# Kernel tuning notes

Measured on AMD Instinct MI355X. Metric: run time of the kernel, lower is better.

The kernel has to match this reference:

```python
import jax, jax.numpy as jnp
import numpy as np

NUM_HEADS = 8
HIDDEN = 256


def _coattention(qf, rf, Wq, bq, Wk, bk, Wv, bv, Wo, bo, rel_emb):
    # qf, rf: (b, c, h, w); attention is axial over the height axis per width column.
    b, c, h, w = qf.shape
    T = rel_emb.shape[0]  # 2*max(h,w)-1
    q_in = qf.reshape(b, c, h * w).transpose(0, 2, 1)  # b (hw) c
    r_in = rf.reshape(b, c, h * w).transpose(0, 2, 1)
    q = (q_in @ Wq + bq).reshape(b, h, w, NUM_HEADS, HIDDEN).transpose(0, 3, 1, 2, 4)  # b n h w c
    k = (r_in @ Wk + bk).reshape(b, h, w, NUM_HEADS, HIDDEN).transpose(0, 3, 1, 2, 4)
    v = (r_in @ Wv + bv).reshape(b, h, w, NUM_HEADS, HIDDEN).transpose(0, 3, 1, 2, 4)
    scores = jnp.einsum('bnhwc,bnkwc->bnhwk', q, k)
    # relative index table: idx[i, j] = j - i, wrapped like torch negative indexing
    idx_h = (jnp.arange(h)[None, :] - jnp.arange(h)[:, None]) % T  # (h, h)
    idx_w = (jnp.arange(w)[None, :] - jnp.arange(w)[:, None]) % T  # (w, w); h == w required
    rel_h = rel_emb[idx_h]  # (h, h, c)
    rel_w = rel_emb[idx_w]  # (w, w, c)
    scores = scores + jnp.einsum('bnhwc,hkc->bnhwk', q, rel_h)
    scores = scores + jnp.einsum('bnhwc,wkc->bnhwk', q, rel_w)
    probs = jax.nn.softmax(scores / np.float32(np.sqrt(HIDDEN)), axis=-1)
    att = jnp.einsum('bnhwk,bnkwc->bnhwc', probs, v)
    out = att.transpose(0, 2, 3, 1, 4).reshape(b, h * w, NUM_HEADS * HIDDEN)  # b (hw) (n c)
    out = out @ Wo + bo
    return out.transpose(0, 2, 1).reshape(b, c, h, w)


def setup_inputs() -> dict:
    key = jax.random.key(0)
    ks = jax.random.split(key, 8)
    B, C, H, W = 4, 2048, 32, 32
    s = np.float32(0.02)
    return {
        'left_features': jax.random.normal(ks[0], (B, C, H, W), jnp.float32),
        'right_features': jax.random.normal(ks[1], (B, C, H, W), jnp.float32),
        'Wq': jax.random.normal(ks[2], (C, C), jnp.float32) * s,
        'bq': jnp.zeros((C,), jnp.float32),
        'Wk': jax.random.normal(ks[3], (C, C), jnp.float32) * s,
        'bk': jnp.zeros((C,), jnp.float32),
        'Wv': jax.random.normal(ks[4], (C, C), jnp.float32) * s,
        'bv': jnp.zeros((C,), jnp.float32),
        'Wo': jax.random.normal(ks[5], (C, C), jnp.float32) * s,
        'bo': jnp.zeros((C,), jnp.float32),
        'rel_emb': jax.random.normal(ks[6], (2 * max(H, W) - 1, HIDDEN), jnp.float32),
    }


def reference(left_features, right_features, Wq, bq, Wk, bk, Wv, bv, Wo, bo, rel_emb):
    weighted_r = _coattention(left_features, right_features, Wq, bq, Wk, bk, Wv, bv, Wo, bo, rel_emb)
    weighted_l = _coattention(right_features, left_features, Wq, bq, Wk, bk, Wv, bv, Wo, bo, rel_emb)
    left_attended = jnp.concatenate([left_features, weighted_r], axis=1)
    right_attended = jnp.concatenate([right_features, weighted_l], axis=1)
    return (left_attended, right_attended)
```

## Files before the change

kernel.cpp:

```cpp
#include <hip/hip_runtime.h>
#include <hip/hip_bf16.h>

typedef __attribute__((ext_vector_type(8))) short bf16x8;
typedef __attribute__((ext_vector_type(4))) float f32x4;

#define MFMA16(a, b, c) __builtin_amdgcn_mfma_f32_16x16x32_bf16((a), (b), (c), 0, 0, 0)

typedef __attribute__((address_space(1))) const void gconst_t;
typedef __attribute__((address_space(3))) void lds_t;
__device__ __forceinline__ void gload16(const void* gp, void* lp) {
    __builtin_amdgcn_global_load_lds((gconst_t*)gp, (lds_t*)lp, 16, 0, 0);
}

#define BAR() asm volatile("s_barrier" ::: "memory")
#define VMCNT4() asm volatile("s_waitcnt vmcnt(4)" ::: "memory")
#define DRAIN() asm volatile("s_waitcnt vmcnt(0) lgkmcnt(0)" ::: "memory")
#define PRIO1() __builtin_amdgcn_s_setprio(1)
#define PRIO0() __builtin_amdgcn_s_setprio(0)
#define SCHED0() __builtin_amdgcn_sched_barrier(0)

__global__ void transpose_x(const float* __restrict__ in, __hip_bfloat16* __restrict__ out,
                            float* __restrict__ copy_out) {
    __shared__ float tile[32][33];
    int r0 = blockIdx.y * 32, c0 = blockIdx.x * 32;
    size_t zoff = (size_t)blockIdx.z * 2048 * 1024;
    const float* ib = in + zoff;
    __hip_bfloat16* ob = out + zoff;
    float* cb = copy_out + (size_t)blockIdx.z * 4194304;
    int tx = threadIdx.x, ty = threadIdx.y;
#pragma unroll
    for (int i = ty; i < 32; i += 8) {
        float v = ib[(size_t)(r0 + i) * 1024 + c0 + tx];
        tile[i][tx] = v;
        cb[(size_t)(r0 + i) * 1024 + c0 + tx] = v;
    }
    __syncthreads();
#pragma unroll
    for (int i = ty; i < 32; i += 8)
        ob[(size_t)(c0 + i) * 2048 + r0 + tx] = __float2bfloat16(tile[tx][i]);
}

struct TArgs {
    const float* src[4];
    __hip_bfloat16* dst[4];
};
__global__ void transpose_w4(TArgs ta) {
    __shared__ float tile[32][33];
    const int z = blockIdx.z;
    const float* __restrict__ ib = ta.src[z];
    __hip_bfloat16* __restrict__ ob = ta.dst[z];
    int r0 = blockIdx.y * 32, c0 = blockIdx.x * 32;
    int tx = threadIdx.x, ty = threadIdx.y;
#pragma unroll
    for (int i = ty; i < 32; i += 8)
        tile[i][tx] = ib[(size_t)(r0 + i) * 2048 + c0 + tx];
    __syncthreads();
#pragma unroll
    for (int i = ty; i < 32; i += 8)
        ob[(size_t)(c0 + i) * 2048 + r0 + tx] = __float2bfloat16(tile[tx][i]);
}

__global__ void conv_rel(const float* __restrict__ rel, __hip_bfloat16* __restrict__ relb) {
    int i = blockIdx.x * 256 + threadIdx.x;
    if (i < 64 * 256) {
        int r = i >> 8;
        relb[i] = __float2bfloat16(r < 63 ? rel[i] : 0.f);
    }
}

struct GArgs {
    const __hip_bfloat16* A[6];
    const __hip_bfloat16* B[6];
    void* C[6];
    const float* bias[6];
};

template <int MODE>
__global__ __launch_bounds__(512, 2) void gemm8p(GArgs ga, int N, int K,
                                                 float* __restrict__ dout) {
    __shared__ __align__(16) char smem[131072];

    const int gx = gridDim.x, gy = gridDim.y;
    int lid = blockIdx.x + gx * (blockIdx.y + gy * blockIdx.z);
    const int nwg = gx * gy * gridDim.z;
    int swz = (lid & 7) * (nwg >> 3) + (lid >> 3);
    const int z = swz / (gx * gy);
    int rem = swz - z * (gx * gy);
    const int by = rem / gx;
    const int bx = rem - by * gx;

    const __hip_bfloat16* __restrict__ A = ga.A[z];
    const __hip_bfloat16* __restrict__ B = ga.B[z];
    const float* __restrict__ bias = ga.bias[z];
    const int row0 = by * 256, col0 = bx * 256;

    const int tid = threadIdx.x;
    const int wave = tid >> 6, lane = tid & 63;
    const int l15 = lane & 15, lg = lane >> 4;
    const int wm = wave >> 2, wn = wave & 3;

    const int srow = tid >> 3;
    const int sch = (tid & 7) ^ (srow & 7);
    const int xr = (l15 & 7) << 4;
    const int off0 = (lg * 16) ^ xr;
    const int off1 = (64 + lg * 16) ^ xr;
    const int arow = wm * 16384;
    const int brow = 32768 + (wn >> 1) * 16384;
    const int bloc = (wn & 1) * 64;

    f32x4 acc[8][4] = {};
    bf16x8 alo[4][2], ahi[4][2], bhi[2][2], blo0[2][2], blo1[2][2];

    const int NT = K >> 6;
    const int NI = NT >> 1;

    auto STAGE = [&](const __hip_bfloat16* base, int rowb, int T, int bufc, int isB, int h) {
#pragma unroll
        for (int L = 0; L < 2; ++L) {
            const __hip_bfloat16* g =
                base + (size_t)(rowb + h * 128 + L * 64 + srow) * K + T * 64 + sch * 8;
            gload16(g, smem + bufc * 65536 + isB * 32768 + h * 16384 + L * 8192 + wave * 1024);
        }
    };
    auto LDA = [&](int bufc, int mf, int ks) {
        return *(const bf16x8*)(smem + bufc * 65536 + arow + (mf * 16 + l15) * 128 +
                                (ks ? off1 : off0));
    };
    auto LDB = [&](int bufc, int nf, int ks) {
        return *(const bf16x8*)(smem + bufc * 65536 + brow + (bloc + nf * 16 + l15) * 128 +
                                (ks ? off1 : off0));
    };

#define READ_ALO(BUF)                                  \
    _Pragma("unroll") for (int mf = 0; mf < 4; ++mf) { \
        alo[mf][0] = LDA(BUF, mf, 0);                  \
        alo[mf][1] = LDA(BUF, mf, 1);                  \
    }
#define READ_AHI(BUF)                                  \
    _Pragma("unroll") for (int mf = 0; mf < 4; ++mf) { \
        ahi[mf][0] = LDA(BUF, 4 + mf, 0);              \
        ahi[mf][1] = LDA(BUF, 4 + mf, 1);              \
    }
#define READ_BHI(BUF)                                  \
    _Pragma("unroll") for (int nf = 0; nf < 2; ++nf) { \
        bhi[nf][0] = LDB(BUF, 2 + nf, 0);              \
        bhi[nf][1] = LDB(BUF, 2 + nf, 1);              \
    }
#define READ_BLO(BUF, DST)                             \
    _Pragma("unroll") for (int nf = 0; nf < 2; ++nf) { \
        DST[nf][0] = LDB(BUF, nf, 0);                  \
        DST[nf][1] = LDB(BUF, nf, 1);                  \
    }
#define MQ(AR, MOFF, NOFF, BR)                                          \
    SCHED0();                                                           \
    PRIO1();                                                            \
    _Pragma("unroll") for (int mf = 0; mf < 4; ++mf)                    \
    _Pragma("unroll") for (int nf = 0; nf < 2; ++nf) {                  \
        acc[(MOFF) + mf][(NOFF) + nf] =                                 \
            MFMA16(AR[mf][0], BR[nf][0], acc[(MOFF) + mf][(NOFF) + nf]); \
        acc[(MOFF) + mf][(NOFF) + nf] =                                 \
            MFMA16(AR[mf][1], BR[nf][1], acc[(MOFF) + mf][(NOFF) + nf]); \
    }                                                                   \
    PRIO0();

    STAGE(B, col0, 0, 0, 1, 0);
    STAGE(A, row0, 0, 0, 0, 0);
    STAGE(A, row0, 0, 0, 0, 1);
    STAGE(B, col0, 0, 0, 1, 1);
    STAGE(B, col0, 1, 1, 1, 0);
    STAGE(A, row0, 1, 1, 0, 0);
    VMCNT4();
    BAR();
    READ_ALO(0);
    READ_BLO(0, blo0);

#pragma unroll 1
    for (int i = 0; i < NI; ++i) {
        const int t = 2 * i;
        const int T2 = (t + 2 < NT) ? t + 2 : t;
        const int T3 = (t + 3 < NT) ? t + 3 : t + 1;
        STAGE(A, row0, t + 1, 1, 0, 1);
        BAR();
        READ_BHI(0);
        MQ(alo, 0, 0, blo0);

        STAGE(B, col0, t + 1, 1, 1, 1);
        BAR();
        READ_AHI(0);
        MQ(alo, 0, 2, bhi);

        STAGE(B, col0, T2, 0, 1, 0);
        BAR();
        MQ(ahi, 4, 2, bhi);

        STAGE(A, row0, T2, 0, 0, 0);
        VMCNT4();
        BAR();
        READ_ALO(1);
        READ_BLO(1, blo1);
        MQ(ahi, 4, 0, blo0);

        STAGE(A, row0, T2, 0, 0, 1);
        BAR();
        READ_BHI(1);
        MQ(alo, 0, 0, blo1);

        STAGE(B, col0, T2, 0, 1, 1);
        BAR();
        READ_AHI(1);
        MQ(alo, 0, 2, bhi);

        STAGE(B, col0, T3, 1, 1, 0);
        BAR();
        MQ(ahi, 4, 2, bhi);

        STAGE(A, row0, T3, 1, 0, 0);
        VMCNT4();
        BAR();
        READ_ALO(0);
        READ_BLO(0, blo0);
        MQ(ahi, 4, 0, blo1);
    }
    DRAIN();

    if (MODE == 0) {
        __hip_bfloat16* __restrict__ C = (__hip_bfloat16*)ga.C[z];
#pragma unroll
        for (int mf = 0; mf < 8; ++mf) {
            int m = row0 + wm * 128 + mf * 16 + lg * 4;
#pragma unroll
            for (int nf = 0; nf < 4; ++nf) {
                int n = col0 + wn * 64 + nf * 16 + l15;
                float bv = bias[n];
#pragma unroll
                for (int r = 0; r < 4; ++r)
                    C[(size_t)(m + r) * N + n] = __float2bfloat16(acc[mf][nf][r] + bv);
            }
        }
    } else {
        float* __restrict__ OB = dout + (size_t)z * 16777216;
#pragma unroll
        for (int mf = 0; mf < 8; ++mf) {
            int n0 = row0 + wm * 128 + mf * 16 + lg * 4;
#pragma unroll
            for (int nf = 0; nf < 4; ++nf) {
                int m = col0 + wn * 64 + nf * 16 + l15;
                size_t base = (size_t)(m >> 10) * 4194304 + (size_t)(m & 1023);
#pragma unroll
                for (int r = 0; r < 4; ++r) {
                    int n = n0 + r;
                    OB[base + (size_t)(2048 + n) * 1024] = acc[mf][nf][r] + bias[n];
                }
            }
        }
    }
#undef READ_ALO
#undef READ_AHI
#undef READ_BHI
#undef READ_BLO
#undef MQ
}

__global__ __launch_bounds__(256, 2) void attn_kernel(
    const __hip_bfloat16* __restrict__ Qa, const __hip_bfloat16* __restrict__ Ka,
    const __hip_bfloat16* __restrict__ Va, const __hip_bfloat16* __restrict__ Qb,
    const __hip_bfloat16* __restrict__ Kb, const __hip_bfloat16* __restrict__ Vb,
    const __hip_bfloat16* __restrict__ relb, __hip_bfloat16* __restrict__ Oa,
    __hip_bfloat16* __restrict__ Ob) {
    const int w = blockIdx.x;
    const int nh = blockIdx.y;
    const int zb = blockIdx.z;
    const int dir = zb >> 2, b = zb & 3;
    const __hip_bfloat16* __restrict__ Q = dir ? Qb : Qa;
    const __hip_bfloat16* __restrict__ K = dir ? Kb : Ka;
    const __hip_bfloat16* __restrict__ V = dir ? Vb : Va;
    __hip_bfloat16* __restrict__ O = dir ? Ob : Oa;

    __shared__ __align__(16) __hip_bfloat16 vt[256 * 40];
    __shared__ float ssc[32 * 32];
    __shared__ float es[32 * 64];
    __shared__ __align__(16) __hip_bfloat16 ps[32 * 32];

    const int tid = threadIdx.x;
    const int lane = tid & 63, wave = tid >> 6;
    const int l15 = lane & 15, lg = lane >> 4;
    const int mt = wave >> 1, nt = wave & 1;

    const size_t rowbase = ((size_t)b * 1024 + w) * 2048 + (size_t)nh * 256;

    for (int i = 0; i < 32; ++i) {
        int e = i * 256 + tid;
        int hk = e >> 8, c = e & 255;
        vt[c * 40 + hk] = V[rowbase + (size_t)hk * 65536 + c];
    }

    f32x4 sacc = {}, e0 = {}, e1 = {};
#pragma unroll
    for (int k8 = 0; k8 < 256; k8 += 32) {
        bf16x8 af = *(const bf16x8*)&Q[rowbase + (size_t)(mt * 16 + l15) * 65536 + k8 + lg * 8];
        bf16x8 bf = *(const bf16x8*)&K[rowbase + (size_t)(nt * 16 + l15) * 65536 + k8 + lg * 8];
        bf16x8 r0 = *(const bf16x8*)&relb[(size_t)(nt * 32 + l15) * 256 + k8 + lg * 8];
        bf16x8 r1 = *(const bf16x8*)&relb[(size_t)(nt * 32 + 16 + l15) * 256 + k8 + lg * 8];
        sacc = MFMA16(af, bf, sacc);
        e0 = MFMA16(af, r0, e0);
        e1 = MFMA16(af, r1, e1);
    }
#pragma unroll
    for (int r = 0; r < 4; ++r) {
        int row = mt * 16 + lg * 4 + r;
        ssc[row * 32 + nt * 16 + l15] = sacc[r];
        es[row * 64 + nt * 32 + l15] = e0[r];
        es[row * 64 + nt * 32 + 16 + l15] = e1[r];
    }
    __syncthreads();

    {
        int h = tid >> 3, sub = tid & 7;
        float v4[4];
        float mx = -1e30f;
#pragma unroll
        for (int i = 0; i < 4; ++i) {
            int k = sub * 4 + i;
            int dh = k - h; if (dh < 0) dh += 63;
            int dw = k - w; if (dw < 0) dw += 63;
            float s = (ssc[h * 32 + k] + es[h * 64 + dh] + es[h * 64 + dw]) * 0.0625f;
            v4[i] = s;
            mx = fmaxf(mx, s);
        }
        mx = fmaxf(mx, __shfl_xor(mx, 1));
        mx = fmaxf(mx, __shfl_xor(mx, 2));
        mx = fmaxf(mx, __shfl_xor(mx, 4));
        float sum = 0.f;
#pragma unroll
        for (int i = 0; i < 4; ++i) {
            v4[i] = __expf(v4[i] - mx);
            sum += v4[i];
        }
        sum += __shfl_xor(sum, 1);
        sum += __shfl_xor(sum, 2);
        sum += __shfl_xor(sum, 4);
        float inv = 1.f / sum;
#pragma unroll
        for (int i = 0; i < 4; ++i) ps[h * 32 + sub * 4 + i] = __float2bfloat16(v4[i] * inv);
    }
    __syncthreads();

    bf16x8 paf = *(const bf16x8*)&ps[(mt * 16 + l15) * 32 + lg * 8];
#pragma unroll
    for (int j = 0; j < 8; ++j) {
        int ct = nt * 8 + j;
        bf16x8 bv = *(const bf16x8*)&vt[(size_t)(ct * 16 + l15) * 40 + lg * 8];
        f32x4 oacc = {};
        oacc = MFMA16(paf, bv, oacc);
#pragma unroll
        for (int r = 0; r < 4; ++r) {
            int hh = mt * 16 + lg * 4 + r;
            O[rowbase + (size_t)hh * 65536 + ct * 16 + l15] = __float2bfloat16(oacc[r]);
        }
    }
}

extern "C" void kernel_launch(void* const* d_in, const int* in_sizes, int n_in, void* d_out,
                              int out_size, void* d_ws, size_t ws_size, hipStream_t stream) {
    const float* Xl = (const float*)d_in[0];
    const float* Xr = (const float*)d_in[1];
    const float* Wq = (const float*)d_in[2];
    const float* bq = (const float*)d_in[3];
    const float* Wk = (const float*)d_in[4];
    const float* bk = (const float*)d_in[5];
    const float* Wv = (const float*)d_in[6];
    const float* bv = (const float*)d_in[7];
    const float* Wo = (const float*)d_in[8];
    const float* bo = (const float*)d_in[9];
    const float* rel = (const float*)d_in[10];
    float* out = (float*)d_out;

    char* ws = (char*)d_ws;
    size_t off = 0;
    auto nxt = [&](size_t bytes) {
        void* p = ws + off;
        off += bytes;
        return p;
    };
    __hip_bfloat16* Xbl = (__hip_bfloat16*)nxt(16777216);
    __hip_bfloat16* Xbr = (__hip_bfloat16*)nxt(16777216);
    __hip_bfloat16* Wtq = (__hip_bfloat16*)nxt(8388608);
    __hip_bfloat16* Wtk = (__hip_bfloat16*)nxt(8388608);
    __hip_bfloat16* Wtv = (__hip_bfloat16*)nxt(8388608);
    __hip_bfloat16* Wto = (__hip_bfloat16*)nxt(8388608);
    __hip_bfloat16* relb = (__hip_bfloat16*)nxt(32768);
    __hip_bfloat16* Ql = (__hip_bfloat16*)nxt(16777216);
    __hip_bfloat16* Kl = (__hip_bfloat16*)nxt(16777216);
    __hip_bfloat16* Vl = (__hip_bfloat16*)nxt(16777216);
    __hip_bfloat16* Qr = (__hip_bfloat16*)nxt(16777216);
    __hip_bfloat16* Kr = (__hip_bfloat16*)nxt(16777216);
    __hip_bfloat16* Vr = (__hip_bfloat16*)nxt(16777216);
    __hip_bfloat16* At0 = Xbl;
    __hip_bfloat16* At1 = Xbr;

    dim3 tb(32, 8);
    transpose_x<<<dim3(32, 64, 4), tb, 0, stream>>>(Xl, Xbl, out);
    transpose_x<<<dim3(32, 64, 4), tb, 0, stream>>>(Xr, Xbr, out + 16777216);
    TArgs tw;
    tw.src[0] = Wq; tw.src[1] = Wk; tw.src[2] = Wv; tw.src[3] = Wo;
    tw.dst[0] = Wtq; tw.dst[1] = Wtk; tw.dst[2] = Wtv; tw.dst[3] = Wto;
    transpose_w4<<<dim3(64, 64, 4), tb, 0, stream>>>(tw);
    conv_rel<<<64, 256, 0, stream>>>(rel, relb);

    GArgs g1 = {};
    g1.A[0] = Xbl; g1.A[1] = Xbl; g1.A[2] = Xbl;
    g1.A[3] = Xbr; g1.A[4] = Xbr; g1.A[5] = Xbr;
    g1.B[0] = Wtq; g1.B[1] = Wtk; g1.B[2] = Wtv;
    g1.B[3] = Wtq; g1.B[4] = Wtk; g1.B[5] = Wtv;
    g1.C[0] = Ql; g1.C[1] = Kl; g1.C[2] = Vl;
    g1.C[3] = Qr; g1.C[4] = Kr; g1.C[5] = Vr;
    g1.bias[0] = bq; g1.bias[1] = bk; g1.bias[2] = bv;
    g1.bias[3] = bq; g1.bias[4] = bk; g1.bias[5] = bv;
    gemm8p<0><<<dim3(8, 16, 6), 512, 0, stream>>>(g1, 2048, 2048, nullptr);

    attn_kernel<<<dim3(32, 8, 8), 256, 0, stream>>>(Ql, Kr, Vr, Qr, Kl, Vl, relb, At0, At1);

    GArgs g2 = {};
    g2.A[0] = Wto; g2.A[1] = Wto;
    g2.B[0] = At0; g2.B[1] = At1;
    g2.bias[0] = bo; g2.bias[1] = bo;
    gemm8p<1><<<dim3(16, 8, 2), 512, 0, stream>>>(g2, 2048, 2048, out);
}
```

Before: 386.7 us.

## Load GEMM B operand directly from global into registers, stage only A in LDS

Restructures the GEMM main loop so that only the A tile is staged through LDS (halving shared memory to 64KB), while each wave loads its B fragments directly from global memory into registers, double-buffered across k-steps. The previous 8-phase interleaved schedule with partial vmcnt waits is replaced by a simpler per-tile window that issues the next loads, does LDS reads and MFMAs, then waits for all loads and barriers. This aims to cut LDS traffic and capacity and to simplify synchronisation. The costs are uncoalesced global B loads, duplicate B reads across waves (wm=0/1), a full vmcnt(0) stall each tile, and higher register pressure.

Result: slower. 488.5 us (+26.3%).

```diff
diff --git a/kernel.cpp b/kernel.cpp
--- a/kernel.cpp
+++ b/kernel.cpp
@@ -13,8 +13,7 @@
 }
 
 #define BAR() asm volatile("s_barrier" ::: "memory")
-#define VMCNT4() asm volatile("s_waitcnt vmcnt(4)" ::: "memory")
-#define DRAIN() asm volatile("s_waitcnt vmcnt(0) lgkmcnt(0)" ::: "memory")
+#define VMCNT0() asm volatile("s_waitcnt vmcnt(0)" ::: "memory")
 #define PRIO1() __builtin_amdgcn_s_setprio(1)
 #define PRIO0() __builtin_amdgcn_s_setprio(0)
 #define SCHED0() __builtin_amdgcn_sched_barrier(0)
@@ -78,7 +77,7 @@
 template <int MODE>
 __global__ __launch_bounds__(512, 2) void gemm8p(GArgs ga, int N, int K,
                                                  float* __restrict__ dout) {
-    __shared__ __align__(16) char smem[131072];
+    __shared__ __align__(16) char smem[65536];
 
     const int gx = gridDim.x, gy = gridDim.y;
     int lid = blockIdx.x + gx * (blockIdx.y + gy * blockIdx.z);
@@ -102,126 +101,78 @@
     const int srow = tid >> 3;
     const int sch = (tid & 7) ^ (srow & 7);
     const int xr = (l15 & 7) << 4;
-    const int off0 = (lg * 16) ^ xr;
-    const int off1 = (64 + lg * 16) ^ xr;
-    const int arow = wm * 16384;
-    const int brow = 32768 + (wn >> 1) * 16384;
-    const int bloc = (wn & 1) * 64;
+
+    const __hip_bfloat16* Bw = B + (size_t)(col0 + wn * 64) * K;
 
     f32x4 acc[8][4] = {};
-    bf16x8 alo[4][2], ahi[4][2], bhi[2][2], blo0[2][2], blo1[2][2];
+    bf16x8 bA[4][2], bB[4][2], a0[2][2], a1[2][2];
 
     const int NT = K >> 6;
-    const int NI = NT >> 1;
-
-    auto STAGE = [&](const __hip_bfloat16* base, int rowb, int T, int bufc, int isB, int h) {
-#pragma unroll
-        for (int L = 0; L < 2; ++L) {
+
+    auto STAGE = [&](int T, int bufsel) {
+#pragma unroll
+        for (int L = 0; L < 4; ++L) {
             const __hip_bfloat16* g =
-                base + (size_t)(rowb + h * 128 + L * 64 + srow) * K + T * 64 + sch * 8;
-            gload16(g, smem + bufc * 65536 + isB * 32768 + h * 16384 + L * 8192 + wave * 1024);
+                A + (size_t)(row0 + L * 64 + srow) * K + T * 64 + sch * 8;
+            gload16(g, smem + bufsel * 32768 + L * 8192 + wave * 1024);
         }
     };
-    auto LDA = [&](int bufc, int mf, int ks) {
-        return *(const bf16x8*)(smem + bufc * 65536 + arow + (mf * 16 + l15) * 128 +
-                                (ks ? off1 : off0));
+    auto BLOAD = [&](bf16x8 (&dst)[4][2], int T) {
+#pragma unroll
+        for (int nf = 0; nf < 4; ++nf)
+#pragma unroll
+            for (int ks = 0; ks < 2; ++ks)
+                dst[nf][ks] =
+                    *(const bf16x8*)&Bw[(size_t)(nf * 16 + l15) * K + T * 64 + ks * 32 + lg * 8];
     };
-    auto LDB = [&](int bufc, int nf, int ks) {
-        return *(const bf16x8*)(smem + bufc * 65536 + brow + (bloc + nf * 16 + l15) * 128 +
-                                (ks ? off1 : off0));
+    auto RDA = [&](bf16x8 (&dst)[2][2], int bufsel, int mf0) {
+#pragma unroll
+        for (int p = 0; p < 2; ++p)
+#pragma unroll
+            for (int ks = 0; ks < 2; ++ks) {
+                int row = wm * 128 + (mf0 + p) * 16 + l15;
+                dst[p][ks] = *(const bf16x8*)(smem + bufsel * 32768 + row * 128 +
+                                              ((ks * 64 + lg * 16) ^ xr));
+            }
     };
 
-#define READ_ALO(BUF)                                  \
-    _Pragma("unroll") for (int mf = 0; mf < 4; ++mf) { \
-        alo[mf][0] = LDA(BUF, mf, 0);                  \
-        alo[mf][1] = LDA(BUF, mf, 1);                  \
-    }
-#define READ_AHI(BUF)                                  \
-    _Pragma("unroll") for (int mf = 0; mf < 4; ++mf) { \
-        ahi[mf][0] = LDA(BUF, 4 + mf, 0);              \
-        ahi[mf][1] = LDA(BUF, 4 + mf, 1);              \
-    }
-#define READ_BHI(BUF)                                  \
-    _Pragma("unroll") for (int nf = 0; nf < 2; ++nf) { \
-        bhi[nf][0] = LDB(BUF, 2 + nf, 0);              \
-        bhi[nf][1] = LDB(BUF, 2 + nf, 1);              \
-    }
-#define READ_BLO(BUF, DST)                             \
-    _Pragma("unroll") for (int nf = 0; nf < 2; ++nf) { \
-        DST[nf][0] = LDB(BUF, nf, 0);                  \
-        DST[nf][1] = LDB(BUF, nf, 1);                  \
-    }
-#define MQ(AR, MOFF, NOFF, BR)                                          \
-    SCHED0();                                                           \
-    PRIO1();                                                            \
-    _Pragma("unroll") for (int mf = 0; mf < 4; ++mf)                    \
-    _Pragma("unroll") for (int nf = 0; nf < 2; ++nf) {                  \
-        acc[(MOFF) + mf][(NOFF) + nf] =                                 \
-            MFMA16(AR[mf][0], BR[nf][0], acc[(MOFF) + mf][(NOFF) + nf]); \
-        acc[(MOFF) + mf][(NOFF) + nf] =                                 \
-            MFMA16(AR[mf][1], BR[nf][1], acc[(MOFF) + mf][(NOFF) + nf]); \
-    }                                                                   \
-    PRIO0();
-
-    STAGE(B, col0, 0, 0, 1, 0);
-    STAGE(A, row0, 0, 0, 0, 0);
-    STAGE(A, row0, 0, 0, 0, 1);
-    STAGE(B, col0, 0, 0, 1, 1);
-    STAGE(B, col0, 1, 1, 1, 0);
-    STAGE(A, row0, 1, 1, 0, 0);
-    VMCNT4();
+#define MFMA2(AP, MOFF, BC)                                                       \
+    _Pragma("unroll") for (int p = 0; p < 2; ++p)                                 \
+    _Pragma("unroll") for (int nf = 0; nf < 4; ++nf) {                            \
+        acc[(MOFF) + p][nf] = MFMA16(AP[p][0], BC[nf][0], acc[(MOFF) + p][nf]);   \
+        acc[(MOFF) + p][nf] = MFMA16(AP[p][1], BC[nf][1], acc[(MOFF) + p][nf]);   \
+    }
+
+#define WINDOW(TT, BUFSEL, BC, BN)                            \
+    {                                                         \
+        const int tn = ((TT) + 1 < NT) ? (TT) + 1 : (TT);     \
+        STAGE(tn, (BUFSEL) ^ 1);                              \
+        BLOAD(BN, tn);                                        \
+        SCHED0();                                             \
+        RDA(a0, (BUFSEL), 0);                                 \
+        RDA(a1, (BUFSEL), 2);                                 \
+        PRIO1();                                              \
+        MFMA2(a0, 0, BC);                                     \
+        RDA(a0, (BUFSEL), 4);                                 \
+        MFMA2(a1, 2, BC);                                     \
+        RDA(a1, (BUFSEL), 6);                                 \
+        MFMA2(a0, 4, BC);                                     \
+        MFMA2(a1, 6, BC);                                     \
+        PRIO0();                                              \
+        VMCNT0();                                             \
+        BAR();                                                \
+    }
+
+    STAGE(0, 0);
+    BLOAD(bA, 0);
+    VMCNT0();
     BAR();
-    READ_ALO(0);
-    READ_BLO(0, blo0);
 
 #pragma unroll 1
-    for (int i = 0; i < NI; ++i) {
-        const int t = 2 * i;
-        const int T2 = (t + 2 < NT) ? t + 2 : t;
-        const int T3 = (t + 3 < NT) ? t + 3 : t + 1;
-        STAGE(A, row0, t + 1, 1, 0, 1);
-        BAR();
-        READ_BHI(0);
-        MQ(alo, 0, 0, blo0);
-
-        STAGE(B, col0, t + 1, 1, 1, 1);
-        BAR();
-        READ_AHI(0);
-        MQ(alo, 0, 2, bhi);
-
-        STAGE(B, col0, T2, 0, 1, 0);
-        BAR();
-        MQ(ahi, 4, 2, bhi);
-
-        STAGE(A, row0, T2, 0, 0, 0);
-        VMCNT4();
-        BAR();
-        READ_ALO(1);
-        READ_BLO(1, blo1);
-        MQ(ahi, 4, 0, blo0);
-
-        STAGE(A, row0, T2, 0, 0, 1);
-        BAR();
-        READ_BHI(1);
-        MQ(alo, 0, 0, blo1);
-
-        STAGE(B, col0, T2, 0, 1, 1);
-        BAR();
-        READ_AHI(1);
-        MQ(alo, 0, 2, bhi);
-
-        STAGE(B, col0, T3, 1, 1, 0);
-        BAR();
-        MQ(ahi, 4, 2, bhi);
-
-        STAGE(A, row0, T3, 1, 0, 0);
-        VMCNT4();
-        BAR();
-        READ_ALO(0);
-        READ_BLO(0, blo0);
-        MQ(ahi, 4, 0, blo1);
-    }
-    DRAIN();
+    for (int t = 0; t < NT; t += 2) {
+        WINDOW(t, 0, bA, bB);
+        WINDOW(t + 1, 1, bB, bA);
+    }
 
     if (MODE == 0) {
         __hip_bfloat16* __restrict__ C = (__hip_bfloat16*)ga.C[z];
@@ -254,11 +205,8 @@
             }
         }
     }
-#undef READ_ALO
-#undef READ_AHI
-#undef READ_BHI
-#undef READ_BLO
-#undef MQ
+#undef MFMA2
+#undef WINDOW
 }
 
 __global__ __launch_bounds__(256, 2) void attn_kernel(
```
